# Performance work log

Measured on AMD Instinct MI355X. Metric: run time of the kernel, lower is better.

The kernel has to match this reference:

```python
import jax, jax.numpy as jnp
import numpy as np

N = 4096
IN_DIM = 256
H = 4        # n_heads
D = 64       # head_dim (out_dim)
NEG_SLOPE = 0.2


def setup_inputs() -> dict:
    key = jax.random.key(0)
    k_h, k_adj, k_zero, k_W, k_a = jax.random.split(key, 5)
    h = jax.random.normal(k_h, (N, IN_DIM), dtype=jnp.float32)
    adj = jax.random.normal(k_adj, (N, N), dtype=jnp.float32)
    keep = jax.random.uniform(k_zero, (N, N)) >= 0.3
    adj_bias = jnp.where(keep, adj, 0.0)
    W = jax.random.normal(k_W, (IN_DIM, H * D), dtype=jnp.float32) * 0.05
    a = jax.random.normal(k_a, (H, 2 * D), dtype=jnp.float32) * 0.05
    return {"h": h, "adj_bias": adj_bias, "W": W, "a": a}


def reference(h, adj_bias, W, a):
    n = h.shape[0]
    Wh = (h @ W).reshape(n, H, D)                       # [N, H, D]
    # (cat([Wh_i, Wh_j]) * a).sum(-1) separates into two rank-1 terms:
    a_i, a_j = a[:, :D], a[:, D:]                       # [H, D] each
    e_i = jnp.einsum('nhd,hd->nh', Wh, a_i)             # score from dest node i
    e_j = jnp.einsum('nhd,hd->nh', Wh, a_j)             # score from src node j
    e = jax.nn.leaky_relu(e_i[:, None, :] + e_j[None, :, :], NEG_SLOPE)  # [N,N,H]
    mask = (adj_bias == 0.0)[:, :, None]                # [N, N, 1]
    e = e + adj_bias[:, :, None]
    e = jnp.where(mask, -jnp.inf, e)
    # rows where every neighbor is masked: force self-loop score 0
    all_masked = jnp.all(mask, axis=1, keepdims=True)   # [N, 1, 1]
    self_loop = jnp.eye(n, dtype=bool)[:, :, None]      # [N, N, 1]
    e = jnp.where(all_masked & self_loop, 0.0, e)
    alpha = jax.nn.softmax(e, axis=1)                   # softmax over sources j
    # dropout: eval mode (p acts as identity), faithful to training=False
    out = jnp.einsum('ijh,jhd->ihd', alpha, Wh).reshape(n, H * D)  # concat heads
    return jax.nn.elu(out)
```

## Files before the change

### kernel.cpp

```cpp
#include <hip/hip_runtime.h>
#include <cstdint>
#include <cstddef>


typedef _Float16 f16x2 __attribute__((ext_vector_type(2)));
typedef _Float16 f16x4 __attribute__((ext_vector_type(4)));
typedef _Float16 f16x8 __attribute__((ext_vector_type(8)));
typedef float f32x4 __attribute__((ext_vector_type(4)));

#define NN 4096

__global__ __launch_bounds__(256) void gemm_wh(
    const float* __restrict__ A, const float* __restrict__ Bw,
    const float* __restrict__ av, float* __restrict__ C,
    _Float16* __restrict__ Vt,
    _Float16* __restrict__ uit, _Float16* __restrict__ ui5t,
    _Float16* __restrict__ ujt, _Float16* __restrict__ uj5t) {
  __shared__ float sA[32][36];
  __shared__ float sB[32][68];
  __shared__ _Float16 sT[64][40];
  const int h  = blockIdx.x;
  const int by = blockIdx.y;
  const int t  = threadIdx.x;
  const int row0 = by * 32, col0 = h * 64;
  const int tc = t & 15, tr = t >> 4;
  float acc[2][4];
  #pragma unroll
  for (int q = 0; q < 2; q++)
    #pragma unroll
    for (int p = 0; p < 4; p++) acc[q][p] = 0.f;

  for (int k0 = 0; k0 < 256; k0 += 32) {
    __syncthreads();
    {
      const int r = t >> 3, k4 = (t & 7) * 4;
      float4 v = *(const float4*)&A[(size_t)(row0 + r) * 256 + k0 + k4];
      sA[k4 + 0][r] = v.x; sA[k4 + 1][r] = v.y;
      sA[k4 + 2][r] = v.z; sA[k4 + 3][r] = v.w;
    }
    #pragma unroll
    for (int q = 0; q < 2; q++) {
      const int u = t + q * 256;
      const int kr = u >> 4, c4 = (u & 15) * 4;
      *(float4*)&sB[kr][c4] =
          *(const float4*)&Bw[(size_t)(k0 + kr) * 256 + col0 + c4];
    }
    __syncthreads();
    #pragma unroll
    for (int kk = 0; kk < 32; kk++) {
      float2 a2 = *(const float2*)&sA[kk][tr * 2];
      float4 bv = *(const float4*)&sB[kk][tc * 4];
      const float bp[4] = {bv.x, bv.y, bv.z, bv.w};
      #pragma unroll
      for (int p = 0; p < 4; p++) {
        acc[0][p] = fmaf(a2.x, bp[p], acc[0][p]);
        acc[1][p] = fmaf(a2.y, bp[p], acc[1][p]);
      }
    }
  }
  #pragma unroll
  for (int q = 0; q < 2; q++) {
    float4 v = make_float4(acc[q][0], acc[q][1], acc[q][2], acc[q][3]);
    *(float4*)&C[(size_t)(row0 + tr * 2 + q) * 256 + col0 + tc * 4] = v;
  }
  {
    float pi[2] = {0.f, 0.f}, pj[2] = {0.f, 0.f};
    #pragma unroll
    for (int q = 0; q < 2; q++)
      #pragma unroll
      for (int p = 0; p < 4; p++) {
        const int d = tc * 4 + p;
        pi[q] = fmaf(acc[q][p], av[h * 128 + d], pi[q]);
        pj[q] = fmaf(acc[q][p], av[h * 128 + 64 + d], pj[q]);
      }
    #pragma unroll
    for (int m = 1; m <= 8; m <<= 1) {
      #pragma unroll
      for (int q = 0; q < 2; q++) {
        pi[q] += __shfl_xor(pi[q], m, 64);
        pj[q] += __shfl_xor(pj[q], m, 64);
      }
    }
    if (tc == 0) {
      #pragma unroll
      for (int q = 0; q < 2; q++) {
        const int row = row0 + tr * 2 + q;
        uit [(size_t)h * NN + row] = (_Float16)__expf(0.2f * pi[q]);
        ui5t[(size_t)h * NN + row] = (_Float16)__expf(pi[q]);
        ujt [(size_t)h * NN + row] = (_Float16)__expf(0.2f * pj[q]);
        uj5t[(size_t)h * NN + row] = (_Float16)__expf(pj[q]);
      }
    }
  }
  #pragma unroll
  for (int q = 0; q < 2; q++)
    #pragma unroll
    for (int p = 0; p < 4; p++)
      sT[tc * 4 + p][tr * 2 + q] = (_Float16)acc[q][p];
  __syncthreads();
  {
    const int dd = t >> 2, j8 = (t & 3) * 8;
    f16x8 w;
    #pragma unroll
    for (int k = 0; k < 8; k++) w[k] = sT[dd][j8 + k];
    *(f16x8*)&Vt[(size_t)(col0 + dd) * NN + row0 + j8] = w;
  }
}

__global__ __launch_bounds__(256, 4) void gat_attn(
    const float* __restrict__ bias, const _Float16* __restrict__ Vt,
    const _Float16* __restrict__ uit, const _Float16* __restrict__ ui5t,
    const _Float16* __restrict__ ujt, const _Float16* __restrict__ uj5t,
    float* __restrict__ P, float* __restrict__ L, int jpc) {
  __shared__ float rawb[32][128];
  __shared__ _Float16 seb[2][32][136];
  const int itile = blockIdx.x;
  const int chunk = blockIdx.y;
  const int tid = threadIdx.x;
  const int lane = tid & 63;
  const int h = __builtin_amdgcn_readfirstlane(tid >> 6);
  const int m = lane & 15;
  const int quad = lane >> 4;
  const int i0 = itile * 32;
  const int j0 = chunk * jpc;
  const int nc = jpc >> 7;

  f32x4 acc[2][5];
  #pragma unroll
  for (int it = 0; it < 2; it++)
    #pragma unroll
    for (int dt = 0; dt < 5; dt++)
      #pragma unroll
      for (int r = 0; r < 4; r++) acc[it][dt][r] = 0.f;

  const _Float16 ui_0 = uit [(size_t)h * NN + i0 + m];
  const _Float16 ui_1 = uit [(size_t)h * NN + i0 + 16 + m];
  const _Float16 u5_0 = ui5t[(size_t)h * NN + i0 + m];
  const _Float16 u5_1 = ui5t[(size_t)h * NN + i0 + 16 + m];
  const f16x8 ui8_0 = {ui_0, ui_0, ui_0, ui_0, ui_0, ui_0, ui_0, ui_0};
  const f16x8 ui8_1 = {ui_1, ui_1, ui_1, ui_1, ui_1, ui_1, ui_1, ui_1};
  const f16x8 u58_0 = {u5_0, u5_0, u5_0, u5_0, u5_0, u5_0, u5_0, u5_0};
  const f16x8 u58_1 = {u5_1, u5_1, u5_1, u5_1, u5_1, u5_1, u5_1, u5_1};
  const f16x8 kOne = {(_Float16)1.f, (_Float16)1.f, (_Float16)1.f, (_Float16)1.f,
                      (_Float16)1.f, (_Float16)1.f, (_Float16)1.f, (_Float16)1.f};

  const int lr = (h << 3) + (lane >> 5);
  const int lc = lane & 31;
  const float* gb = bias + (size_t)(i0 + lr) * NN + j0 + lc * 4;

  auto issue_load = [&](int jc) {
    const float* g = gb + jc * 128;
    #pragma unroll
    for (int q = 0; q < 4; q++) {
      __builtin_amdgcn_global_load_lds(
          (const __attribute__((address_space(1))) uint32_t*)(g + (size_t)(q * 2) * NN),
          (__attribute__((address_space(3))) uint32_t*)&rawb[(h << 3) + q * 2][0],
          16, 0, 0);
    }
  };
  auto convert = [&](int buf) {
    #pragma unroll
    for (int rr = 0; rr < 8; rr++) {
      const int r = (h << 3) + rr;
      const float2 v = *(const float2*)&rawb[r][lane * 2];
      f16x2 e;
      e[0] = (_Float16)((v.x == 0.f) ? 0.f : __expf(v.x));
      e[1] = (_Float16)((v.y == 0.f) ? 0.f : __expf(v.y));
      *(f16x2*)&seb[buf][r][lane * 2] = e;
    }
  };

  issue_load(0);
  __syncthreads();
  convert(0);

  for (int jc = 0; jc < nc; jc++) {
    const int buf = jc & 1;
    __syncthreads();
    if (jc + 1 < nc) issue_load(jc + 1);

    const _Float16* vb  = Vt + (size_t)(h * 64 + m) * NN + j0 + jc * 128 + quad * 8;
    const _Float16* ujb = ujt  + (size_t)h * NN + j0 + jc * 128 + quad * 8;
    const _Float16* u5b = uj5t + (size_t)h * NN + j0 + jc * 128 + quad * 8;

    #pragma unroll
    for (int s = 0; s < 4; s++) {
      f16x8 bc[4];
      #pragma unroll
      for (int dt = 0; dt < 4; dt++)
        bc[dt] = *(const f16x8*)(vb + (size_t)(dt * 16) * NN + s * 32);
      const f16x8 uj8  = *(const f16x8*)(ujb + s * 32);
      const f16x8 uj58 = *(const f16x8*)(u5b + s * 32);
      const f16x8 e0 = *(const f16x8*)&seb[buf][m][s * 32 + quad * 8];
      const f16x8 e1 = *(const f16x8*)&seb[buf][m + 16][s * 32 + quad * 8];
      const f16x8 a0 = e0 * __builtin_elementwise_max(u58_0 * uj58, ui8_0 * uj8);
      const f16x8 a1 = e1 * __builtin_elementwise_max(u58_1 * uj58, ui8_1 * uj8);
      __builtin_amdgcn_s_setprio(1);
      #pragma unroll
      for (int dt = 0; dt < 4; dt++) {
        acc[0][dt] = __builtin_amdgcn_mfma_f32_16x16x32_f16(a0, bc[dt], acc[0][dt], 0, 0, 0);
        acc[1][dt] = __builtin_amdgcn_mfma_f32_16x16x32_f16(a1, bc[dt], acc[1][dt], 0, 0, 0);
      }
      acc[0][4] = __builtin_amdgcn_mfma_f32_16x16x32_f16(a0, kOne, acc[0][4], 0, 0, 0);
      acc[1][4] = __builtin_amdgcn_mfma_f32_16x16x32_f16(a1, kOne, acc[1][4], 0, 0, 0);
      __builtin_amdgcn_s_setprio(0);
    }

    __syncthreads();
    if (jc + 1 < nc) convert(buf ^ 1);
  }

  const size_t lb = (size_t)(chunk * 4 + h) * NN + i0;
  if (m == 0) {
    #pragma unroll
    for (int it = 0; it < 2; it++)
      #pragma unroll
      for (int r = 0; r < 4; r++)
        L[lb + it * 16 + quad * 4 + r] = acc[it][4][r];
  }
  const size_t pbase = ((size_t)(chunk * 4 + h) * NN + i0) * 64;
  #pragma unroll
  for (int it = 0; it < 2; it++)
    #pragma unroll
    for (int dt = 0; dt < 4; dt++)
      #pragma unroll
      for (int r = 0; r < 4; r++)
        P[pbase + (size_t)(it * 16 + quad * 4 + r) * 64 + dt * 16 + m] = acc[it][dt][r];
}

template <int CHT>
__global__ __launch_bounds__(256) void reduce_out(
    const float* __restrict__ P, const float* __restrict__ L,
    const float* __restrict__ Wh, float* __restrict__ out) {
  const int i0 = blockIdx.x * 16;
  const int h = blockIdx.y;
  const int t = threadIdx.x;
  const int d2 = (t & 31) * 2;
  const int isub = t >> 5;
  #pragma unroll
  for (int ii = 0; ii < 2; ii++) {
    const int i = i0 + isub * 2 + ii;
    float lsum = 0.f;
    float sx = 0.f, sy = 0.f;
    #pragma unroll
    for (int c = 0; c < CHT; c++) {
      lsum += L[(size_t)(c * 4 + h) * NN + i];
      const float2 p = *(const float2*)&P[((size_t)(c * 4 + h) * NN + i) * 64 + d2];
      sx += p.x; sy += p.y;
    }
    const float2 wh = *(const float2*)&Wh[(size_t)i * 256 + h * 64 + d2];
    const bool fb = (lsum == 0.f);
    float ox = fb ? wh.x : sx / lsum;
    float oy = fb ? wh.y : sy / lsum;
    ox = (ox > 0.f) ? ox : (__expf(ox) - 1.f);
    oy = (oy > 0.f) ? oy : (__expf(oy) - 1.f);
    float2 o = make_float2(ox, oy);
    *(float2*)&out[(size_t)i * 256 + h * 64 + d2] = o;
  }
}

extern "C" void kernel_launch(void* const* d_in, const int* in_sizes, int n_in,
                              void* d_out, int out_size, void* d_ws, size_t ws_size,
                              hipStream_t stream) {
  const float* h_in = (const float*)d_in[0];
  const float* adj  = (const float*)d_in[1];
  const float* W    = (const float*)d_in[2];
  const float* a    = (const float*)d_in[3];
  float* out = (float*)d_out;
  float* ws = (float*)d_ws;

  int CH = 8;
  while (CH > 1) {
    size_t floats = 1048576  + 524288  + 32768  +
                    (size_t)CH * (16384 + 1048576);
    if (floats * 4 <= ws_size) break;
    CH >>= 1;
  }
  const int jpc = NN / CH;

  float* Wh = ws;
  _Float16* Vt   = (_Float16*)(ws + 1048576);
  _Float16* uit  = (_Float16*)(ws + 1048576 + 524288);
  _Float16* ui5t = uit + 16384;
  _Float16* ujt  = ui5t + 16384;
  _Float16* uj5t = ujt + 16384;
  float* Lb = ws + 1048576 + 524288 + 32768;
  float* Pb = Lb + (size_t)CH * 16384;

  hipLaunchKernelGGL(gemm_wh, dim3(4, 128), dim3(256), 0, stream,
                     h_in, W, a, Wh, Vt, uit, ui5t, ujt, uj5t);
  hipLaunchKernelGGL(gat_attn, dim3(128, CH), dim3(256), 0, stream,
                     adj, Vt, uit, ui5t, ujt, uj5t, Pb, Lb, jpc);
  switch (CH) {
    case 8: hipLaunchKernelGGL((reduce_out<8>), dim3(256, 4), dim3(256), 0, stream, Pb, Lb, Wh, out); break;
    case 4: hipLaunchKernelGGL((reduce_out<4>), dim3(256, 4), dim3(256), 0, stream, Pb, Lb, Wh, out); break;
    case 2: hipLaunchKernelGGL((reduce_out<2>), dim3(256, 4), dim3(256), 0, stream, Pb, Lb, Wh, out); break;
    default: hipLaunchKernelGGL((reduce_out<1>), dim3(256, 4), dim3(256), 0, stream, Pb, Lb, Wh, out); break;
  }
}
```

Baseline: 158.3 us.

## Precompute exp(adj_bias) as fp16 in GEMM kernel and stream it into attention

The GEMM kernel now also converts the full fp32 adjacency-bias matrix into an fp16 matrix of exp(bias), with masked entries set to zero. A new attention kernel reads this half-size matrix directly from global memory instead of staging fp32 bias through shared memory and computing exponentials per head. This halves the bytes the attention pass reads and removes the repeated per-head exp work and LDS staging. The cost is an extra full N×N read and fp16 write pass inside the GEMM kernel, plus 32 MB of extra workspace, with a fallback to the old path when the workspace is too small.

```diff
diff --git a/kernel.cpp b/kernel.cpp
--- a/kernel.cpp
+++ b/kernel.cpp
@@ -15,7 +15,8 @@
     const float* __restrict__ av, float* __restrict__ C,
     _Float16* __restrict__ Vt,
     _Float16* __restrict__ uit, _Float16* __restrict__ ui5t,
-    _Float16* __restrict__ ujt, _Float16* __restrict__ uj5t) {
+    _Float16* __restrict__ ujt, _Float16* __restrict__ uj5t,
+    const float* __restrict__ bsrc, _Float16* __restrict__ ebp) {
   __shared__ float sA[32][36];
   __shared__ float sB[32][68];
   __shared__ _Float16 sT[64][40];
@@ -105,6 +106,111 @@
     for (int k = 0; k < 8; k++) w[k] = sT[dd][j8 + k];
     *(f16x8*)&Vt[(size_t)(col0 + dd) * NN + row0 + j8] = w;
   }
+  if (ebp != nullptr) {
+    const size_t base = ((size_t)blockIdx.x * 128 + blockIdx.y) * 32768;
+    #pragma unroll 4
+    for (int k = 0; k < 16; k++) {
+      const size_t idx = base + (size_t)k * 2048 + (size_t)t * 8;
+      const float4 v0 = *(const float4*)&bsrc[idx];
+      const float4 v1 = *(const float4*)&bsrc[idx + 4];
+      f16x8 e;
+      e[0] = (_Float16)((v0.x == 0.f) ? 0.f : __expf(v0.x));
+      e[1] = (_Float16)((v0.y == 0.f) ? 0.f : __expf(v0.y));
+      e[2] = (_Float16)((v0.z == 0.f) ? 0.f : __expf(v0.z));
+      e[3] = (_Float16)((v0.w == 0.f) ? 0.f : __expf(v0.w));
+      e[4] = (_Float16)((v1.x == 0.f) ? 0.f : __expf(v1.x));
+      e[5] = (_Float16)((v1.y == 0.f) ? 0.f : __expf(v1.y));
+      e[6] = (_Float16)((v1.z == 0.f) ? 0.f : __expf(v1.z));
+      e[7] = (_Float16)((v1.w == 0.f) ? 0.f : __expf(v1.w));
+      *(f16x8*)&ebp[idx] = e;
+    }
+  }
+}
+
+__global__ __launch_bounds__(256, 4) void gat_attn_eb(
+    const _Float16* __restrict__ eb, const _Float16* __restrict__ Vt,
+    const _Float16* __restrict__ uit, const _Float16* __restrict__ ui5t,
+    const _Float16* __restrict__ ujt, const _Float16* __restrict__ uj5t,
+    float* __restrict__ P, float* __restrict__ L, int jpc) {
+  const int itile = blockIdx.x;
+  const int chunk = blockIdx.y;
+  const int tid = threadIdx.x;
+  const int lane = tid & 63;
+  const int h = __builtin_amdgcn_readfirstlane(tid >> 6);
+  const int m = lane & 15;
+  const int quad = lane >> 4;
+  const int i0 = itile * 32;
+  const int j0 = chunk * jpc;
+  const int nc = jpc >> 7;
+
+  f32x4 acc[2][5];
+  #pragma unroll
+  for (int it = 0; it < 2; it++)
+    #pragma unroll
+    for (int dt = 0; dt < 5; dt++)
+      #pragma unroll
+      for (int r = 0; r < 4; r++) acc[it][dt][r] = 0.f;
+
+  const _Float16 ui_0 = uit [(size_t)h * NN + i0 + m];
+  const _Float16 ui_1 = uit [(size_t)h * NN + i0 + 16 + m];
+  const _Float16 u5_0 = ui5t[(size_t)h * NN + i0 + m];
+  const _Float16 u5_1 = ui5t[(size_t)h * NN + i0 + 16 + m];
+  const f16x8 ui8_0 = {ui_0, ui_0, ui_0, ui_0, ui_0, ui_0, ui_0, ui_0};
+  const f16x8 ui8_1 = {ui_1, ui_1, ui_1, ui_1, ui_1, ui_1, ui_1, ui_1};
+  const f16x8 u58_0 = {u5_0, u5_0, u5_0, u5_0, u5_0, u5_0, u5_0, u5_0};
+  const f16x8 u58_1 = {u5_1, u5_1, u5_1, u5_1, u5_1, u5_1, u5_1, u5_1};
+  const f16x8 kOne = {(_Float16)1.f, (_Float16)1.f, (_Float16)1.f, (_Float16)1.f,
+                      (_Float16)1.f, (_Float16)1.f, (_Float16)1.f, (_Float16)1.f};
+
+  const _Float16* e0p = eb + (size_t)(i0 + m) * NN + j0 + quad * 8;
+  const _Float16* e1p = e0p + (size_t)16 * NN;
+  const _Float16* vb  = Vt + (size_t)(h * 64 + m) * NN + j0 + quad * 8;
+  const _Float16* ujb = ujt  + (size_t)h * NN + j0 + quad * 8;
+  const _Float16* u5b = uj5t + (size_t)h * NN + j0 + quad * 8;
+
+  for (int jc = 0; jc < nc; jc++) {
+    const int jb = jc * 128;
+    #pragma unroll
+    for (int s = 0; s < 4; s++) {
+      const int off = jb + s * 32;
+      const f16x8 e0   = *(const f16x8*)(e0p + off);
+      const f16x8 e1   = *(const f16x8*)(e1p + off);
+      const f16x8 uj8  = *(const f16x8*)(ujb + off);
+      const f16x8 uj58 = *(const f16x8*)(u5b + off);
+      f16x8 bc[4];
+      #pragma unroll
+      for (int dt = 0; dt < 4; dt++)
+        bc[dt] = *(const f16x8*)(vb + (size_t)(dt * 16) * NN + off);
+      const f16x8 a0 = e0 * __builtin_elementwise_max(u58_0 * uj58, ui8_0 * uj8);
+      const f16x8 a1 = e1 * __builtin_elementwise_max(u58_1 * uj58, ui8_1 * uj8);
+      __builtin_amdgcn_s_setprio(1);
+      #pragma unroll
+      for (int dt = 0; dt < 4; dt++) {
+        acc[0][dt] = __builtin_amdgcn_mfma_f32_16x16x32_f16(a0, bc[dt], acc[0][dt], 0, 0, 0);
+        acc[1][dt] = __builtin_amdgcn_mfma_f32_16x16x32_f16(a1, bc[dt], acc[1][dt], 0, 0, 0);
+      }
+      acc[0][4] = __builtin_amdgcn_mfma_f32_16x16x32_f16(a0, kOne, acc[0][4], 0, 0, 0);
+      acc[1][4] = __builtin_amdgcn_mfma_f32_16x16x32_f16(a1, kOne, acc[1][4], 0, 0, 0);
+      __builtin_amdgcn_s_setprio(0);
+    }
+  }
+
+  const size_t lb = (size_t)(chunk * 4 + h) * NN + i0;
+  if (m == 0) {
+    #pragma unroll
+    for (int it = 0; it < 2; it++)
+      #pragma unroll
+      for (int r = 0; r < 4; r++)
+        L[lb + it * 16 + quad * 4 + r] = acc[it][4][r];
+  }
+  const size_t pbase = ((size_t)(chunk * 4 + h) * NN + i0) * 64;
+  #pragma unroll
+  for (int it = 0; it < 2; it++)
+    #pragma unroll
+    for (int dt = 0; dt < 4; dt++)
+      #pragma unroll
+      for (int r = 0; r < 4; r++)
+        P[pbase + (size_t)(it * 16 + quad * 4 + r) * 64 + dt * 16 + m] = acc[it][dt][r];
 }
 
 __global__ __launch_bounds__(256, 4) void gat_attn(
@@ -269,12 +375,16 @@
   float* out = (float*)d_out;
   float* ws = (float*)d_ws;
 
+  const size_t kFixed0 = 1048576 + 524288 + 32768;
+  const size_t kEb = 8388608;
+  const size_t kPerCh = 16384 + 1048576;
+
   int CH = 8;
-  while (CH > 1) {
-    size_t floats = 1048576  + 524288  + 32768  +
-                    (size_t)CH * (16384 + 1048576);
-    if (floats * 4 <= ws_size) break;
-    CH >>= 1;
+  while (CH > 1 && (kFixed0 + kEb + (size_t)CH * kPerCh) * 4 > ws_size) CH >>= 1;
+  bool use_eb = (kFixed0 + kEb + (size_t)CH * kPerCh) * 4 <= ws_size;
+  if (!use_eb) {
+    CH = 8;
+    while (CH > 1 && (kFixed0 + (size_t)CH * kPerCh) * 4 > ws_size) CH >>= 1;
   }
   const int jpc = NN / CH;
 
@@ -284,13 +394,19 @@
   _Float16* ui5t = uit + 16384;
   _Float16* ujt  = ui5t + 16384;
   _Float16* uj5t = ujt + 16384;
-  float* Lb = ws + 1048576 + 524288 + 32768;
+  _Float16* ebp  = use_eb ? (_Float16*)(ws + kFixed0) : nullptr;
+  float* Lb = ws + kFixed0 + (use_eb ? kEb : 0);
   float* Pb = Lb + (size_t)CH * 16384;
 
   hipLaunchKernelGGL(gemm_wh, dim3(4, 128), dim3(256), 0, stream,
-                     h_in, W, a, Wh, Vt, uit, ui5t, ujt, uj5t);
-  hipLaunchKernelGGL(gat_attn, dim3(128, CH), dim3(256), 0, stream,
-                     adj, Vt, uit, ui5t, ujt, uj5t, Pb, Lb, jpc);
+                     h_in, W, a, Wh, Vt, uit, ui5t, ujt, uj5t, adj, ebp);
+  if (use_eb) {
+    hipLaunchKernelGGL(gat_attn_eb, dim3(128, CH), dim3(256), 0, stream,
+                       ebp, Vt, uit, ui5t, ujt, uj5t, Pb, Lb, jpc);
+  } else {
+    hipLaunchKernelGGL(gat_attn, dim3(128, CH), dim3(256), 0, stream,
+                       adj, Vt, uit, ui5t, ujt, uj5t, Pb, Lb, jpc);
+  }
   switch (CH) {
     case 8: hipLaunchKernelGGL((reduce_out<8>), dim3(256, 4), dim3(256), 0, stream, Pb, Lb, Wh, out); break;
     case 4: hipLaunchKernelGGL((reduce_out<4>), dim3(256, 4), dim3(256), 0, stream, Pb, Lb, Wh, out); break;
```

Result: slower. 174.6 us (+10.3%).

## Double gat_attn row tile to 64 and software-prefetch operands across k-steps

Applied to the files above, without the earlier changes.

Each gat_attn block now covers 64 destination rows instead of 32, so every V tile and uj vector loaded from global memory feeds four MFMA row tiles instead of two, halving the number of blocks and the redundant V reads. Inside each 128-column chunk, the operands for the next 32-column step are loaded before the current MFMAs issue, to hide load latency. The larger register footprint (20 accumulators plus prefetch buffers) and doubled LDS size are handled by lowering the occupancy hint to 2 blocks, which risks less latency hiding and fewer blocks to fill the GPU.

```diff
diff --git a/kernel.cpp b/kernel.cpp
--- a/kernel.cpp
+++ b/kernel.cpp
@@ -107,13 +107,13 @@
   }
 }
 
-__global__ __launch_bounds__(256, 4) void gat_attn(
+__global__ __launch_bounds__(256, 2) void gat_attn(
     const float* __restrict__ bias, const _Float16* __restrict__ Vt,
     const _Float16* __restrict__ uit, const _Float16* __restrict__ ui5t,
     const _Float16* __restrict__ ujt, const _Float16* __restrict__ uj5t,
     float* __restrict__ P, float* __restrict__ L, int jpc) {
-  __shared__ float rawb[32][128];
-  __shared__ _Float16 seb[2][32][136];
+  __shared__ float rawb[64][128];
+  __shared__ _Float16 seb[2][64][136];
   const int itile = blockIdx.x;
   const int chunk = blockIdx.y;
   const int tid = threadIdx.x;
@@ -121,47 +121,47 @@
   const int h = __builtin_amdgcn_readfirstlane(tid >> 6);
   const int m = lane & 15;
   const int quad = lane >> 4;
-  const int i0 = itile * 32;
+  const int i0 = itile * 64;
   const int j0 = chunk * jpc;
   const int nc = jpc >> 7;
 
-  f32x4 acc[2][5];
-  #pragma unroll
-  for (int it = 0; it < 2; it++)
+  f32x4 acc[4][5];
+  #pragma unroll
+  for (int it = 0; it < 4; it++)
     #pragma unroll
     for (int dt = 0; dt < 5; dt++)
       #pragma unroll
       for (int r = 0; r < 4; r++) acc[it][dt][r] = 0.f;
 
-  const _Float16 ui_0 = uit [(size_t)h * NN + i0 + m];
-  const _Float16 ui_1 = uit [(size_t)h * NN + i0 + 16 + m];
-  const _Float16 u5_0 = ui5t[(size_t)h * NN + i0 + m];
-  const _Float16 u5_1 = ui5t[(size_t)h * NN + i0 + 16 + m];
-  const f16x8 ui8_0 = {ui_0, ui_0, ui_0, ui_0, ui_0, ui_0, ui_0, ui_0};
-  const f16x8 ui8_1 = {ui_1, ui_1, ui_1, ui_1, ui_1, ui_1, ui_1, ui_1};
-  const f16x8 u58_0 = {u5_0, u5_0, u5_0, u5_0, u5_0, u5_0, u5_0, u5_0};
-  const f16x8 u58_1 = {u5_1, u5_1, u5_1, u5_1, u5_1, u5_1, u5_1, u5_1};
+  f16x8 ui8[4], u58[4];
+  #pragma unroll
+  for (int it = 0; it < 4; it++) {
+    const _Float16 u1 = uit [(size_t)h * NN + i0 + it * 16 + m];
+    const _Float16 u5 = ui5t[(size_t)h * NN + i0 + it * 16 + m];
+    ui8[it] = (f16x8){u1, u1, u1, u1, u1, u1, u1, u1};
+    u58[it] = (f16x8){u5, u5, u5, u5, u5, u5, u5, u5};
+  }
   const f16x8 kOne = {(_Float16)1.f, (_Float16)1.f, (_Float16)1.f, (_Float16)1.f,
                       (_Float16)1.f, (_Float16)1.f, (_Float16)1.f, (_Float16)1.f};
 
-  const int lr = (h << 3) + (lane >> 5);
+  const int lr = h * 16 + (lane >> 5);
   const int lc = lane & 31;
   const float* gb = bias + (size_t)(i0 + lr) * NN + j0 + lc * 4;
 
   auto issue_load = [&](int jc) {
     const float* g = gb + jc * 128;
     #pragma unroll
-    for (int q = 0; q < 4; q++) {
+    for (int q = 0; q < 8; q++) {
       __builtin_amdgcn_global_load_lds(
           (const __attribute__((address_space(1))) uint32_t*)(g + (size_t)(q * 2) * NN),
-          (__attribute__((address_space(3))) uint32_t*)&rawb[(h << 3) + q * 2][0],
+          (__attribute__((address_space(3))) uint32_t*)&rawb[h * 16 + q * 2][0],
           16, 0, 0);
     }
   };
   auto convert = [&](int buf) {
     #pragma unroll
-    for (int rr = 0; rr < 8; rr++) {
-      const int r = (h << 3) + rr;
+    for (int rr = 0; rr < 16; rr++) {
+      const int r = h * 16 + rr;
       const float2 v = *(const float2*)&rawb[r][lane * 2];
       f16x2 e;
       e[0] = (_Float16)((v.x == 0.f) ? 0.f : __expf(v.x));
@@ -174,36 +174,60 @@
   __syncthreads();
   convert(0);
 
+  const _Float16* vb  = Vt + (size_t)(h * 64 + m) * NN + j0 + quad * 8;
+  const _Float16* ujb = ujt  + (size_t)h * NN + j0 + quad * 8;
+  const _Float16* u5b = uj5t + (size_t)h * NN + j0 + quad * 8;
+
   for (int jc = 0; jc < nc; jc++) {
     const int buf = jc & 1;
     __syncthreads();
     if (jc + 1 < nc) issue_load(jc + 1);
 
-    const _Float16* vb  = Vt + (size_t)(h * 64 + m) * NN + j0 + jc * 128 + quad * 8;
-    const _Float16* ujb = ujt  + (size_t)h * NN + j0 + jc * 128 + quad * 8;
-    const _Float16* u5b = uj5t + (size_t)h * NN + j0 + jc * 128 + quad * 8;
+    const int jb = jc * 128;
+    f16x8 bc[4], ec[4], ujc, u5c;
+    #pragma unroll
+    for (int dt = 0; dt < 4; dt++)
+      bc[dt] = *(const f16x8*)(vb + (size_t)(dt * 16) * NN + jb);
+    ujc = *(const f16x8*)(ujb + jb);
+    u5c = *(const f16x8*)(u5b + jb);
+    #pragma unroll
+    for (int it = 0; it < 4; it++)
+      ec[it] = *(const f16x8*)&seb[buf][it * 16 + m][quad * 8];
 
     #pragma unroll
     for (int s = 0; s < 4; s++) {
-      f16x8 bc[4];
-      #pragma unroll
-      for (int dt = 0; dt < 4; dt++)
-        bc[dt] = *(const f16x8*)(vb + (size_t)(dt * 16) * NN + s * 32);
-      const f16x8 uj8  = *(const f16x8*)(ujb + s * 32);
-      const f16x8 uj58 = *(const f16x8*)(u5b + s * 32);
-      const f16x8 e0 = *(const f16x8*)&seb[buf][m][s * 32 + quad * 8];
-      const f16x8 e1 = *(const f16x8*)&seb[buf][m + 16][s * 32 + quad * 8];
-      const f16x8 a0 = e0 * __builtin_elementwise_max(u58_0 * uj58, ui8_0 * uj8);
-      const f16x8 a1 = e1 * __builtin_elementwise_max(u58_1 * uj58, ui8_1 * uj8);
+      f16x8 bn[4], en[4], ujn, u5n;
+      if (s < 3) {
+        const int off = jb + (s + 1) * 32;
+        #pragma unroll
+        for (int dt = 0; dt < 4; dt++)
+          bn[dt] = *(const f16x8*)(vb + (size_t)(dt * 16) * NN + off);
+        ujn = *(const f16x8*)(ujb + off);
+        u5n = *(const f16x8*)(u5b + off);
+        #pragma unroll
+        for (int it = 0; it < 4; it++)
+          en[it] = *(const f16x8*)&seb[buf][it * 16 + m][(s + 1) * 32 + quad * 8];
+      }
+      f16x8 a[4];
+      #pragma unroll
+      for (int it = 0; it < 4; it++)
+        a[it] = ec[it] * __builtin_elementwise_max(u58[it] * u5c, ui8[it] * ujc);
       __builtin_amdgcn_s_setprio(1);
       #pragma unroll
-      for (int dt = 0; dt < 4; dt++) {
-        acc[0][dt] = __builtin_amdgcn_mfma_f32_16x16x32_f16(a0, bc[dt], acc[0][dt], 0, 0, 0);
-        acc[1][dt] = __builtin_amdgcn_mfma_f32_16x16x32_f16(a1, bc[dt], acc[1][dt], 0, 0, 0);
-      }
-      acc[0][4] = __builtin_amdgcn_mfma_f32_16x16x32_f16(a0, kOne, acc[0][4], 0, 0, 0);
-      acc[1][4] = __builtin_amdgcn_mfma_f32_16x16x32_f16(a1, kOne, acc[1][4], 0, 0, 0);
+      for (int it = 0; it < 4; it++) {
+        #pragma unroll
+        for (int dt = 0; dt < 4; dt++)
+          acc[it][dt] = __builtin_amdgcn_mfma_f32_16x16x32_f16(a[it], bc[dt], acc[it][dt], 0, 0, 0);
+        acc[it][4] = __builtin_amdgcn_mfma_f32_16x16x32_f16(a[it], kOne, acc[it][4], 0, 0, 0);
+      }
       __builtin_amdgcn_s_setprio(0);
+      if (s < 3) {
+        #pragma unroll
+        for (int dt = 0; dt < 4; dt++) bc[dt] = bn[dt];
+        #pragma unroll
+        for (int it = 0; it < 4; it++) ec[it] = en[it];
+        ujc = ujn; u5c = u5n;
+      }
     }
 
     __syncthreads();
@@ -213,14 +237,14 @@
   const size_t lb = (size_t)(chunk * 4 + h) * NN + i0;
   if (m == 0) {
     #pragma unroll
-    for (int it = 0; it < 2; it++)
+    for (int it = 0; it < 4; it++)
       #pragma unroll
       for (int r = 0; r < 4; r++)
         L[lb + it * 16 + quad * 4 + r] = acc[it][4][r];
   }
   const size_t pbase = ((size_t)(chunk * 4 + h) * NN + i0) * 64;
   #pragma unroll
-  for (int it = 0; it < 2; it++)
+  for (int it = 0; it < 4; it++)
     #pragma unroll
     for (int dt = 0; dt < 4; dt++)
       #pragma unroll
@@ -289,7 +313,7 @@
 
   hipLaunchKernelGGL(gemm_wh, dim3(4, 128), dim3(256), 0, stream,
                      h_in, W, a, Wh, Vt, uit, ui5t, ujt, uj5t);
-  hipLaunchKernelGGL(gat_attn, dim3(128, CH), dim3(256), 0, stream,
+  hipLaunchKernelGGL(gat_attn, dim3(64, CH), dim3(256), 0, stream,
                      adj, Vt, uit, ui5t, ujt, uj5t, Pb, Lb, jpc);
   switch (CH) {
     case 8: hipLaunchKernelGGL((reduce_out<8>), dim3(256, 4), dim3(256), 0, stream, Pb, Lb, Wh, out); break;
```

Result: faster. 144.1 us, median of 2 (-8.9%).
